# Kernel optimization log

Hardware: AMD Instinct MI355X
Metric: run time of the kernel (lower is better)

Reference implementation:

```python
import jax, jax.numpy as jnp
import numpy as np


def setup_inputs() -> dict:
    key = jax.random.key(0)
    k1, k2, k3 = jax.random.split(key, 3)
    B, S, D, E, H = 4, 2048, 1024, 8, 1024
    x = jax.random.normal(k1, (B, S, D), dtype=jnp.float32)
    Wg = jax.random.normal(k2, (D, E), dtype=jnp.float32) / np.sqrt(D)
    We = jax.random.normal(k3, (E, D, H), dtype=jnp.float32) / np.sqrt(D)
    be = jnp.zeros((E, H), dtype=jnp.float32)
    return {"x": x, "Wg": Wg, "We": We, "be": be}


def reference(x, Wg, We, be):
    B, S, D = x.shape
    E = Wg.shape[1]
    T = B * S
    xf = x.reshape(T, D)
    # Top-2 gating (softmax over experts, renormalize the chosen 2)
    gates = jax.nn.softmax(xf @ Wg, axis=-1)                 # [T, E]
    top_g, top_i = jax.lax.top_k(gates, 2)                   # [T, 2]
    top_g = top_g / jnp.sum(top_g, axis=-1, keepdims=True)
    # Dense dispatch matrix: dispatch[e, t] = combined gate weight of token t for expert e
    tok = jnp.arange(T)
    dispatch = jnp.zeros((E, T), dtype=gates.dtype)
    for i in range(2):  # fixed top-2, not a data loop
        dispatch = dispatch.at[top_i[:, i], tok].add(top_g[:, i])
    # Per-expert linear (grouped GEMM over all tokens), then weighted combine
    y = jnp.einsum('td,edh->eth', xf, We) + be[:, None, :]   # [E, T, H]
    out = jnp.einsum('et,eth->th', dispatch, y)              # [T, H]
    return out.reshape(B, S, -1)
```

## Files before the change

kernel.cpp:

```cpp
#include <hip/hip_runtime.h>
#include <hip/hip_bf16.h>

#define T_TOK 8192
#define DDIM  1024
#define NEXP  8
#define HDIM  1024
#define SLOT_CAP 17536
#define NCBLK 32

typedef short bf16x8 __attribute__((ext_vector_type(8)));
typedef float f32x4  __attribute__((ext_vector_type(4)));

typedef const __attribute__((address_space(1))) unsigned int* gas_ptr;
typedef __attribute__((address_space(3))) unsigned int*       las_ptr;
#define GLD16(gp, lp) __builtin_amdgcn_global_load_lds((gas_ptr)(gp), (las_ptr)(lp), 16, 0, 0)

static __device__ __forceinline__ unsigned short f2b(float f) {
    union { float f; unsigned int u; } v; v.f = f;
    unsigned int u = v.u;
    u += 0x7fffu + ((u >> 16) & 1u);
    return (unsigned short)(u >> 16);
}
static __device__ __forceinline__ float b2f(unsigned short h) {
    union { unsigned int u; float f; } v; v.u = ((unsigned int)h) << 16;
    return v.f;
}

__global__ __launch_bounds__(256) void moe_routing(
    const float* __restrict__ x, const float* __restrict__ wg,
    unsigned short* __restrict__ xb,
    int* __restrict__ tok_e, float* __restrict__ tok_g)
{
    __shared__ double red[256 * 9];
    __shared__ double part[64];
    __shared__ double lf[NEXP];

    int t   = blockIdx.x;
    int tid = threadIdx.x;

    float4 xv = ((const float4*)(x + (size_t)t * DDIM))[tid];
    ushort4 xs;
    xs.x = f2b(xv.x); xs.y = f2b(xv.y); xs.z = f2b(xv.z); xs.w = f2b(xv.w);
    ((ushort4*)(xb + (size_t)t * DDIM))[tid] = xs;

    double s[NEXP];
    #pragma unroll
    for (int e = 0; e < NEXP; e++) s[e] = 0.0;
    const float* wr = wg + (size_t)tid * 4 * NEXP;
    #pragma unroll
    for (int j = 0; j < 4; j++) {
        double xj = (double)((&xv.x)[j]);
        #pragma unroll
        for (int e = 0; e < NEXP; e++)
            s[e] += xj * (double)wr[j * NEXP + e];
    }
    #pragma unroll
    for (int e = 0; e < NEXP; e++) red[tid * 9 + e] = s[e];
    __syncthreads();

    if (tid < 64) {
        int e = tid >> 3, p = tid & 7;
        double acc = 0.0;
        for (int i = 0; i < 32; i++) acc += red[(i * 8 + p) * 9 + e];
        part[tid] = acc;
    }
    __syncthreads();
    if (tid < NEXP) {
        double acc = 0.0;
        #pragma unroll
        for (int p = 0; p < 8; p++) acc += part[tid * 8 + p];
        lf[tid] = acc;
    }
    __syncthreads();

    if (tid == 0) {
        double l[NEXP];
        #pragma unroll
        for (int e = 0; e < NEXP; e++) l[e] = lf[e];
        int e0 = 0;
        for (int e = 1; e < NEXP; e++) if (l[e] > l[e0]) e0 = e;
        int e1 = (e0 == 0) ? 1 : 0;
        for (int e = 0; e < NEXP; e++) if (e != e0 && l[e] > l[e1]) e1 = e;
        double g0 = 1.0 / (1.0 + exp(l[e1] - l[e0]));
        double g1 = 1.0 - g0;
        tok_e[2*t] = e0; tok_e[2*t+1] = e1;
        tok_g[2*t] = (float)g0; tok_g[2*t+1] = (float)g1;
    }
}

__global__ __launch_bounds__(256) void moe_count(
    const int* __restrict__ tok_e, int* __restrict__ cnt_part)
{
    __shared__ int h[NEXP];
    if (threadIdx.x < NEXP) h[threadIdx.x] = 0;
    __syncthreads();
    int t = blockIdx.x * 256 + threadIdx.x;
    atomicAdd(&h[tok_e[2*t]], 1);
    atomicAdd(&h[tok_e[2*t+1]], 1);
    __syncthreads();
    if (threadIdx.x < NEXP)
        cnt_part[blockIdx.x * NEXP + threadIdx.x] = h[threadIdx.x];
}

__global__ void moe_offsets(const int* __restrict__ cnt_part,
                            int* __restrict__ meta, int* __restrict__ counts,
                            int* __restrict__ cursor) {
    __shared__ int c_s[NEXP];
    int tid = threadIdx.x;
    if (tid < NEXP) {
        int c = 0;
        for (int b = 0; b < NCBLK; b++) c += cnt_part[b * NEXP + tid];
        counts[tid] = c; c_s[tid] = c;
    }
    __syncthreads();
    if (tid == 0) {
        int off = 0;
        for (int e = 0; e < NEXP; e++) {
            meta[e] = off;
            cursor[e] = off;
            off += (c_s[e] + 127) & ~127;
        }
        meta[NEXP] = off;
    }
}

__global__ __launch_bounds__(256) void moe_slotfill(
    const int* __restrict__ tok_e, int* __restrict__ cursor,
    int* __restrict__ slot_token, int* __restrict__ tok_slot)
{
    __shared__ int h[NEXP];
    __shared__ int base[NEXP];
    if (threadIdx.x < NEXP) h[threadIdx.x] = 0;
    __syncthreads();
    int t = blockIdx.x * 256 + threadIdx.x;
    int e0 = tok_e[2*t],     e1 = tok_e[2*t + 1];
    int r0 = atomicAdd(&h[e0], 1);
    int r1 = atomicAdd(&h[e1], 1);
    __syncthreads();
    if (threadIdx.x < NEXP)
        base[threadIdx.x] = atomicAdd(&cursor[threadIdx.x], h[threadIdx.x]);
    __syncthreads();
    int s0 = base[e0] + r0, s1 = base[e1] + r1;
    slot_token[s0] = t;  tok_slot[2*t]     = s0;
    slot_token[s1] = t;  tok_slot[2*t + 1] = s1;
}

__global__ __launch_bounds__(256) void moe_wtrans(
    const float* __restrict__ we, unsigned short* __restrict__ wt)
{
    __shared__ unsigned short tile[64][65];
    int e  = blockIdx.z;
    int d0 = blockIdx.y * 64;
    int h0 = blockIdx.x * 64;
    int c  = threadIdx.x & 63;
    int r4 = threadIdx.x >> 6;
    #pragma unroll
    for (int i = 0; i < 64; i += 4)
        tile[r4 + i][c] = f2b(we[((size_t)e * DDIM + d0 + r4 + i) * HDIM + h0 + c]);
    __syncthreads();
    #pragma unroll
    for (int i = 0; i < 64; i += 4)
        wt[((size_t)e * HDIM + h0 + r4 + i) * DDIM + d0 + c] = tile[c][r4 + i];
}

__global__ __launch_bounds__(256, 4) void moe_gemm(
    const unsigned short* __restrict__ xb,
    const unsigned short* __restrict__ wt,
    const float* __restrict__ be,
    const int* __restrict__ slot_token,
    const int* __restrict__ meta,
    const int* __restrict__ counts,
    unsigned short* __restrict__ y_slot)
{
    __shared__ __align__(16) unsigned short As[3][128 * 32];
    __shared__ __align__(16) unsigned short Bs[2][128 * 32];

    int m0 = blockIdx.y * 128;
    if (m0 >= meta[NEXP]) return;
    int n0 = blockIdx.x * 128;

    int e = 0;
    #pragma unroll
    for (int i = 1; i < NEXP; i++) if (m0 >= meta[i]) e = i;
    int lim = meta[e] + counts[e];

    int tid  = threadIdx.x;
    int lane = tid & 63, wv = tid >> 6;

    int rA = 32 * wv + (lane >> 2);
    int kc = (((lane & 3) ^ ((rA >> 1) & 3)) * 8);
    int sA0 = m0 + rA, sA1 = sA0 + 16;
    int tA0 = (sA0 < lim) ? slot_token[sA0] : 0;
    int tA1 = (sA1 < lim) ? slot_token[sA1] : 0;
    const unsigned short* gA0 = xb + (size_t)tA0 * DDIM + kc;
    const unsigned short* gA1 = xb + (size_t)tA1 * DDIM + kc;
    const unsigned short* gB0 = wt + ((size_t)e * HDIM + n0 + rA) * DDIM + kc;
    const unsigned short* gB1 = gB0 + (size_t)16 * DDIM;
    int c0 = (2 * wv) * 512;
    int c1 = c0 + 512;

    f32x4 acc[4][4];
    #pragma unroll
    for (int i = 0; i < 4; i++)
        #pragma unroll
        for (int j = 0; j < 4; j++) acc[i][j] = (f32x4){0.f, 0.f, 0.f, 0.f};

    int wm = (wv >> 1) * 64, wn = (wv & 1) * 64;
    int l16 = lane & 15, quad = lane >> 4;
    int f = (l16 >> 1) & 3;
    int rdA[4], rdB[4];
    #pragma unroll
    for (int i = 0; i < 4; i++) {
        rdA[i] = (wm + i * 16 + l16) * 32 + ((quad ^ f) * 8);
        rdB[i] = (wn + i * 16 + l16) * 32 + ((quad ^ f) * 8);
    }

#define ISSUE_A(kkv, Ab)                                                      \
    {                                                                         \
        int ko = (kkv) * 32;                                                  \
        GLD16(gA0 + ko, (Ab) + c0);                                           \
        GLD16(gA1 + ko, (Ab) + c1);                                           \
    }
#define ISSUE_B(kkv, Bb)                                                      \
    {                                                                         \
        int ko = (kkv) * 32;                                                  \
        GLD16(gB0 + ko, (Bb) + c0);                                           \
        GLD16(gB1 + ko, (Bb) + c1);                                           \
    }
#define COMPUTE(Ab, Bb)                                                       \
    {                                                                         \
        bf16x8 bfr[4];                                                        \
        _Pragma("unroll")                                                     \
        for (int j = 0; j < 4; j++)                                           \
            bfr[j] = *(const bf16x8*)((Bb) + rdB[j]);                         \
        _Pragma("unroll")                                                     \
        for (int i = 0; i < 4; i++) {                                         \
            bf16x8 af = *(const bf16x8*)((Ab) + rdA[i]);                      \
            _Pragma("unroll")                                                 \
            for (int j = 0; j < 4; j++)                                       \
                acc[i][j] = __builtin_amdgcn_mfma_f32_16x16x32_bf16(          \
                    af, bfr[j], acc[i][j], 0, 0, 0);                          \
        }                                                                     \
    }

    unsigned short *A0 = As[0], *A1 = As[1], *A2 = As[2];
    unsigned short *B0 = Bs[0], *B1 = Bs[1];

    ISSUE_A(0, A0)
    ISSUE_B(0, B0)
    ISSUE_A(1, A1)

    #pragma unroll 1
    for (int kk = 0; kk < 32; ++kk) {
        asm volatile("" ::: "memory");
        if (kk == 31) __builtin_amdgcn_s_waitcnt(0x0F70);
        else          __builtin_amdgcn_s_waitcnt(0x0F72);
        __builtin_amdgcn_s_barrier();
        asm volatile("" ::: "memory");
        COMPUTE(A0, B0)
        if (kk < 31) ISSUE_B(kk + 1, B1)
        if (kk < 30) ISSUE_A(kk + 2, A2)
        unsigned short* tA = A0; A0 = A1; A1 = A2; A2 = tA;
        unsigned short* tB = B0; B0 = B1; B1 = tB;
    }
#undef ISSUE_A
#undef ISSUE_B
#undef COMPUTE

    #pragma unroll
    for (int i = 0; i < 4; i++) {
        #pragma unroll
        for (int r = 0; r < 4; r++) {
            int slot = m0 + wm + i * 16 + quad * 4 + r;
            if (slot >= lim) continue;
            unsigned short* yp = y_slot + (size_t)slot * HDIM + n0;
            #pragma unroll
            for (int j = 0; j < 4; j++) {
                int col = wn + j * 16 + l16;
                yp[col] = f2b(acc[i][j][r] + be[e * HDIM + n0 + col]);
            }
        }
    }
}

__global__ __launch_bounds__(256) void moe_combine(
    const unsigned short* __restrict__ y_slot,
    const int* __restrict__ tok_slot, const float* __restrict__ tok_g,
    float* __restrict__ out)
{
    int t   = blockIdx.x;
    int tid = threadIdx.x;
    int s0 = tok_slot[2 * t], s1 = tok_slot[2 * t + 1];
    float g0 = tok_g[2 * t],  g1 = tok_g[2 * t + 1];
    ushort4 a = ((const ushort4*)(y_slot + (size_t)s0 * HDIM))[tid];
    ushort4 b = ((const ushort4*)(y_slot + (size_t)s1 * HDIM))[tid];
    float4 o;
    o.x = g0 * b2f(a.x) + g1 * b2f(b.x);
    o.y = g0 * b2f(a.y) + g1 * b2f(b.y);
    o.z = g0 * b2f(a.z) + g1 * b2f(b.z);
    o.w = g0 * b2f(a.w) + g1 * b2f(b.w);
    ((float4*)(out + (size_t)t * HDIM))[tid] = o;
}

extern "C" void kernel_launch(void* const* d_in, const int* in_sizes, int n_in,
                              void* d_out, int out_size, void* d_ws, size_t ws_size,
                              hipStream_t stream) {
    const float* x  = (const float*)d_in[0];
    const float* wg = (const float*)d_in[1];
    const float* we = (const float*)d_in[2];
    const float* be = (const float*)d_in[3];
    float* out = (float*)d_out;

    char* ws = (char*)d_ws;
    size_t o = 0;
    auto alloc = [&](size_t bytes) -> void* {
        void* p = ws + o;
        o = (o + bytes + 255) & ~(size_t)255;
        return p;
    };
    unsigned short* xb   = (unsigned short*)alloc((size_t)T_TOK * DDIM * 2);
    unsigned short* wtb  = (unsigned short*)alloc((size_t)NEXP * HDIM * DDIM * 2);
    unsigned short* ysl  = (unsigned short*)alloc((size_t)SLOT_CAP * HDIM * 2);
    int*   slot_token    = (int*)  alloc((size_t)SLOT_CAP * 4);
    int*   cnt_part      = (int*)  alloc((size_t)NCBLK * NEXP * 4);
    int*   counts        = (int*)  alloc(NEXP * 4);
    int*   meta          = (int*)  alloc((NEXP + 1) * 4);
    int*   cursor        = (int*)  alloc(NEXP * 4);
    int*   tok_e         = (int*)  alloc((size_t)T_TOK * 2 * 4);
    float* tok_g         = (float*)alloc((size_t)T_TOK * 2 * 4);
    int*   tok_slot      = (int*)  alloc((size_t)T_TOK * 2 * 4);

    moe_routing<<<T_TOK, 256, 0, stream>>>(x, wg, xb, tok_e, tok_g);
    moe_count<<<NCBLK, 256, 0, stream>>>(tok_e, cnt_part);
    moe_offsets<<<1, 64, 0, stream>>>(cnt_part, meta, counts, cursor);
    moe_slotfill<<<NCBLK, 256, 0, stream>>>(tok_e, cursor, slot_token, tok_slot);
    moe_wtrans<<<dim3(HDIM / 64, DDIM / 64, NEXP), 256, 0, stream>>>(we, wtb);
    moe_gemm<<<dim3(HDIM / 128, SLOT_CAP / 128), 256, 0, stream>>>(
        xb, wtb, be, slot_token, meta, counts, ysl);
    moe_combine<<<T_TOK, 256, 0, stream>>>(ysl, tok_slot, tok_g, out);
}
```

Before: 220.2 us.

## Vectorize gate-weight loads and weight transpose, flatten GEMM grid to 1D

```diff
diff --git a/kernel.cpp b/kernel.cpp
--- a/kernel.cpp
+++ b/kernel.cpp
@@ -46,13 +46,20 @@
     double s[NEXP];
     #pragma unroll
     for (int e = 0; e < NEXP; e++) s[e] = 0.0;
-    const float* wr = wg + (size_t)tid * 4 * NEXP;
+    const float4* wr4 = (const float4*)(wg + (size_t)tid * 4 * NEXP);
     #pragma unroll
     for (int j = 0; j < 4; j++) {
         double xj = (double)((&xv.x)[j]);
-        #pragma unroll
-        for (int e = 0; e < NEXP; e++)
-            s[e] += xj * (double)wr[j * NEXP + e];
+        float4 qa = wr4[2 * j];
+        float4 qb = wr4[2 * j + 1];
+        s[0] += xj * (double)qa.x;
+        s[1] += xj * (double)qa.y;
+        s[2] += xj * (double)qa.z;
+        s[3] += xj * (double)qa.w;
+        s[4] += xj * (double)qb.x;
+        s[5] += xj * (double)qb.y;
+        s[6] += xj * (double)qb.z;
+        s[7] += xj * (double)qb.w;
     }
     #pragma unroll
     for (int e = 0; e < NEXP; e++) red[tid * 9 + e] = s[e];
@@ -148,19 +155,34 @@
 __global__ __launch_bounds__(256) void moe_wtrans(
     const float* __restrict__ we, unsigned short* __restrict__ wt)
 {
-    __shared__ unsigned short tile[64][65];
+    __shared__ unsigned short tile[64 * 66];
     int e  = blockIdx.z;
     int d0 = blockIdx.y * 64;
     int h0 = blockIdx.x * 64;
-    int c  = threadIdx.x & 63;
-    int r4 = threadIdx.x >> 6;
-    #pragma unroll
-    for (int i = 0; i < 64; i += 4)
-        tile[r4 + i][c] = f2b(we[((size_t)e * DDIM + d0 + r4 + i) * HDIM + h0 + c]);
-    __syncthreads();
-    #pragma unroll
-    for (int i = 0; i < 64; i += 4)
-        wt[((size_t)e * HDIM + h0 + r4 + i) * DDIM + d0 + c] = tile[c][r4 + i];
+    int tid = threadIdx.x;
+
+    int dr = tid >> 4;
+    int hc = (tid & 15) * 4;
+    #pragma unroll
+    for (int i = 0; i < 64; i += 16) {
+        float4 v = *(const float4*)(we + ((size_t)e * DDIM + d0 + dr + i) * HDIM + h0 + hc);
+        ushort2 lo; lo.x = f2b(v.x); lo.y = f2b(v.y);
+        ushort2 hi; hi.x = f2b(v.z); hi.y = f2b(v.w);
+        *(ushort2*)&tile[(dr + i) * 66 + hc]     = lo;
+        *(ushort2*)&tile[(dr + i) * 66 + hc + 2] = hi;
+    }
+    __syncthreads();
+
+    int hr = tid >> 2;
+    int dc = (tid & 3) * 16;
+    #pragma unroll
+    for (int sblk = 0; sblk < 2; sblk++) {
+        int db = dc + sblk * 8;
+        union { unsigned short u[8]; bf16x8 v; } r;
+        #pragma unroll
+        for (int i = 0; i < 8; i++) r.u[i] = tile[(db + i) * 66 + hr];
+        *(bf16x8*)(wt + ((size_t)e * HDIM + h0 + hr) * DDIM + d0 + db) = r.v;
+    }
 }
 
 __global__ __launch_bounds__(256, 4) void moe_gemm(
@@ -175,9 +197,10 @@
     __shared__ __align__(16) unsigned short As[3][128 * 32];
     __shared__ __align__(16) unsigned short Bs[2][128 * 32];
 
-    int m0 = blockIdx.y * 128;
+    int bid = blockIdx.x;
+    int m0 = (bid >> 3) * 128;
     if (m0 >= meta[NEXP]) return;
-    int n0 = blockIdx.x * 128;
+    int n0 = (bid & 7) * 128;
 
     int e = 0;
     #pragma unroll
@@ -335,7 +358,7 @@
     moe_offsets<<<1, 64, 0, stream>>>(cnt_part, meta, counts, cursor);
     moe_slotfill<<<NCBLK, 256, 0, stream>>>(tok_e, cursor, slot_token, tok_slot);
     moe_wtrans<<<dim3(HDIM / 64, DDIM / 64, NEXP), 256, 0, stream>>>(we, wtb);
-    moe_gemm<<<dim3(HDIM / 128, SLOT_CAP / 128), 256, 0, stream>>>(
+    moe_gemm<<<8 * (SLOT_CAP / 128), 256, 0, stream>>>(
         xb, wtb, be, slot_token, meta, counts, ysl);
     moe_combine<<<T_TOK, 256, 0, stream>>>(ysl, tok_slot, tok_g, out);
 }
```

Result: no change. 220.5 us (+0.1%).
